# Kernel optimization log

Measured on AMD Instinct MI355X. Metric: run time of the kernel, lower is better.

Reference implementation:

```python
import jax, jax.numpy as jnp
import numpy as np

B, T, L, D, H, E, A, V = 64, 20, 196, 512, 512, 512, 512, 30000


def setup_inputs() -> dict:
    key = jax.random.key(0)
    ks = jax.random.split(key, 20)
    s = 0.02  # param init scale
    inp = {
        "captions": jax.random.randint(ks[0], (B, T), 0, V),
        "image_features": jax.random.normal(ks[1], (B, L, D), dtype=jnp.float32),
        "pooled_features": jax.random.normal(ks[2], (B, H), dtype=jnp.float32),
        "attention_mask": jnp.ones((B, L), dtype=bool),
        # embedding table
        "embedding": jax.random.normal(ks[3], (V, E), dtype=jnp.float32) * s,
        # LSTM (torch gate order i, f, g, o), input = [emb; context]
        "W_ih": jax.random.normal(ks[4], (4 * H, E + H), dtype=jnp.float32) * s,
        "W_hh": jax.random.normal(ks[5], (4 * H, H), dtype=jnp.float32) * s,
        "b_lstm": jnp.zeros((4 * H,), dtype=jnp.float32),
        # additive attention with memory/cell extra query context
        "Wq": jax.random.normal(ks[6], (H, A), dtype=jnp.float32) * s,
        "Wk": jax.random.normal(ks[7], (D, A), dtype=jnp.float32) * s,
        "Wm": jax.random.normal(ks[8], (H, A), dtype=jnp.float32) * s,
        "Wc": jax.random.normal(ks[9], (H, A), dtype=jnp.float32) * s,
        "v_att": jax.random.normal(ks[10], (A,), dtype=jnp.float32) * s,
        # output projection context(H) -> vocab
        "W_out": jax.random.normal(ks[11], (H, V), dtype=jnp.float32) * s,
        "b_out": jnp.zeros((V,), dtype=jnp.float32),
        # hidden/cell init from pooled features (num_layers = 1)
        "W_init_h": jax.random.normal(ks[12], (H, H), dtype=jnp.float32) * s,
        "b_init_h": jnp.zeros((H,), dtype=jnp.float32),
        "W_init_c": jax.random.normal(ks[13], (H, H), dtype=jnp.float32) * s,
        "b_init_c": jnp.zeros((H,), dtype=jnp.float32),
    }
    return inp


def reference(captions, image_features, pooled_features, attention_mask,
              embedding, W_ih, W_hh, b_lstm, Wq, Wk, Wm, Wc, v_att,
              W_out, b_out, W_init_h, b_init_h, W_init_c, b_init_c):
    # init hidden states from pooled features
    h0 = pooled_features @ W_init_h + b_init_h            # [B, H]
    c0 = pooled_features @ W_init_c + b_init_c            # [B, H]
    ctx0 = jnp.zeros_like(h0)                              # prev_context, [B, H]
    emb = embedding[captions]                              # [B, T, E] (dropout = eval identity)
    # precompute key projection once (hoisted out of the timestep loop)
    key_proj = jnp.einsum('bld,da->bla', image_features, Wk)  # [B, L, A]
    neg = jnp.finfo(image_features.dtype).min

    def step(carry, emb_t):
        h, c, ctx = carry
        x = jnp.concatenate([emb_t, ctx], axis=-1)         # [B, E+H]
        gates = x @ W_ih.T + h @ W_hh.T + b_lstm           # [B, 4H]
        i, f, g, o = jnp.split(gates, 4, axis=-1)
        i = jax.nn.sigmoid(i); f = jax.nn.sigmoid(f)
        g = jnp.tanh(g);       o = jax.nn.sigmoid(o)
        c_new = f * c + i * g
        h_new = o * jnp.tanh(c_new)                        # lstm output == query
        # additive attention: query + memory_state(h) + cell_state(c) context
        q = h_new @ Wq + h_new @ Wm + c_new @ Wc           # [B, A]
        scores = jnp.einsum('bla,a->bl', jnp.tanh(key_proj + q[:, None, :]), v_att)
        scores = jnp.where(attention_mask, scores, neg)
        w = jax.nn.softmax(scores, axis=-1)                # [B, L]
        ctx_new = jnp.einsum('bl,bld->bd', w, image_features)  # [B, H]
        logits_t = ctx_new @ W_out + b_out                 # [B, V]
        return (h_new, c_new, ctx_new), logits_t

    _, logits = jax.lax.scan(step, (h0, c0, ctx0), jnp.swapaxes(emb, 0, 1))
    return jnp.swapaxes(logits, 0, 1)  # [B, T, V]
```

## Files before the change

kernel.cpp:

```cpp
#include <hip/hip_runtime.h>
#include <hip/hip_bf16.h>
#include <cstdint>

#define DEV static __device__ __forceinline__

typedef __bf16 bf16;
typedef __bf16 bf16x8 __attribute__((ext_vector_type(8)));
typedef float f32x4 __attribute__((ext_vector_type(4)));

#define B_ 64
#define T_ 20
#define L_ 196
#define E_ 512
#define V_ 30000
#define VPAD 30080
#define XK 2560
#define GN 2048
#define KSPLIT 8
#define KSPAN 10

DEV float sigmoidf_(float x) { return 1.0f / (1.0f + __expf(-x)); }
DEV float tanhf_(float x) { float e = __expf(2.0f * x); return 1.0f - 2.0f / (e + 1.0f); }

DEV float ldf(const void* p, size_t i, int isbf) {
  return isbf ? (float)((const bf16*)p)[i] : ((const float*)p)[i];
}

DEV void gload_lds16(const void* g, void* l) {
  __builtin_amdgcn_global_load_lds(
      (const __attribute__((address_space(1))) void*)(uintptr_t)g,
      (__attribute__((address_space(3))) void*)(uint32_t)(uintptr_t)l,
      16, 0, 0);
}

#define WAITV4_BAR  do { asm volatile("s_waitcnt vmcnt(4)" ::: "memory"); \
                         asm volatile("s_barrier" ::: "memory"); } while (0)
#define WAITV2_BAR  do { asm volatile("s_waitcnt vmcnt(2)" ::: "memory"); \
                         asm volatile("s_barrier" ::: "memory"); } while (0)
#define WAITV0_BAR  do { asm volatile("s_waitcnt vmcnt(0)" ::: "memory"); \
                         asm volatile("s_barrier" ::: "memory"); } while (0)
#define BAR_ONLY    do { asm volatile("s_barrier" ::: "memory"); } while (0)

__global__ void k_detect(const void* __restrict__ emb, int* __restrict__ flag)
{
  if (threadIdx.x == 0) {
    const unsigned* w = (const unsigned*)emb;
    int cnt = 0;
    for (int i = 0; i < 256; ++i) {
      unsigned lo = w[i] & 0xFFFFu;
      unsigned e = (lo >> 7) & 0xFFu;
      if (e >= 100 && e <= 126) ++cnt;
    }
    *flag = (cnt >= 128) ? 1 : 0;
  }
}

__global__ __launch_bounds__(256)
void k_init_mm(const void* __restrict__ pooled, const void* __restrict__ W_init_h,
               const void* __restrict__ W_init_c, float* __restrict__ ipart,
               const int* __restrict__ flag)
{
  const int isbf = *flag;
  const int b = blockIdx.x, ks = blockIdx.y, mat = blockIdx.z;
  const void* W = mat ? W_init_c : W_init_h;
  const int tid = threadIdx.x;
  __shared__ float p_s[64];
  if (tid < 64) p_s[tid] = ldf(pooled, (size_t)b * 512 + ks * 64 + tid, isbf);
  __syncthreads();
  const int kb = ks * 64;
  float a0 = 0.0f, a1 = 0.0f;
#pragma unroll 8
  for (int k = 0; k < 64; ++k) {
    float p = p_s[k];
    a0 += p * ldf(W, (size_t)(kb + k) * 512 + tid, isbf);
    a1 += p * ldf(W, (size_t)(kb + k) * 512 + tid + 256, isbf);
  }
  float* o = ipart + (((size_t)mat * 8 + ks) * 64 + b) * 512;
  o[tid] = a0;
  o[tid + 256] = a1;
}

__global__ __launch_bounds__(256)
void k_pack(const float* __restrict__ ipart, const void* __restrict__ b_init_h,
            const void* __restrict__ b_init_c, const int* __restrict__ captions,
            const void* __restrict__ embedding, const void* __restrict__ Wq,
            const void* __restrict__ Wm, const void* __restrict__ Wc,
            bf16* __restrict__ xcomb, float* __restrict__ c_state,
            bf16* __restrict__ Wqm, bf16* __restrict__ Wcb,
            bf16* __restrict__ hc, const int* __restrict__ flag)
{
  const int isbf = *flag;
  const int tid = threadIdx.x;
  if (blockIdx.x >= 96) {
    size_t base = (size_t)(blockIdx.x - 96) * 8192;
    for (int i = tid; i < 8192; i += 256)
      Wcb[base + i] = (bf16)ldf(Wc, base + i, isbf);
    return;
  }
  if (blockIdx.x >= 64) {
    size_t base = (size_t)(blockIdx.x - 64) * 8192;
    for (int i = tid; i < 8192; i += 256)
      Wqm[base + i] = (bf16)(ldf(Wq, base + i, isbf) + ldf(Wm, base + i, isbf));
    return;
  }
  const int b = blockIdx.x;
  {
    int cap = captions[b * T_];
    for (int i = tid; i < 512; i += 256) {
      xcomb[(size_t)b * XK + i] = (bf16)ldf(embedding, (size_t)cap * E_ + i, isbf);
      xcomb[(size_t)b * XK + 512 + i]  = (bf16)0.0f;
      xcomb[(size_t)b * XK + 1024 + i] = (bf16)0.0f;
    }
  }
#pragma unroll
  for (int jj = 0; jj < 2; ++jj) {
    int j = tid + jj * 256;
    float ah = ldf(b_init_h, j, isbf), ac = ldf(b_init_c, j, isbf);
#pragma unroll
    for (int ks = 0; ks < 8; ++ks) {
      ah += ipart[(((size_t)0 * 8 + ks) * 64 + b) * 512 + j];
      ac += ipart[(((size_t)1 * 8 + ks) * 64 + b) * 512 + j];
    }
    c_state[b * 512 + j] = ac;
    bf16 hh = (bf16)ah;
    bf16 hl = (bf16)(ah - (float)hh);
    bf16 ch = (bf16)ac;
    bf16 cl = (bf16)(ac - (float)ch);
    xcomb[(size_t)b * XK + 1536 + j] = hh;
    xcomb[(size_t)b * XK + 2048 + j] = hl;
    hc[(size_t)b * 2048 + j]        = hh;
    hc[(size_t)b * 2048 + 512 + j]  = hl;
    hc[(size_t)b * 2048 + 1024 + j] = ch;
    hc[(size_t)b * 2048 + 1536 + j] = cl;
  }
}

__global__ __launch_bounds__(256)
void k_gemm(const void* __restrict__ A, const void* __restrict__ Bsrc,
            int N, int K, int kspan, int outmode, int amode, int btmode,
            float* __restrict__ outF, bf16* __restrict__ outB,
            void* __restrict__ outAny, const void* __restrict__ bias,
            const int* __restrict__ flag)
{
  const int isbf = *flag;
  const int tid  = threadIdx.x;
  const int lane = tid & 63, w = tid >> 6;
  const int n0 = blockIdx.x * 64;
  const int yt = blockIdx.y;
  const int m0 = (outmode == 1) ? 0 : yt * 64;
  const int kbase = (outmode == 1) ? yt * kspan * 32 : 0;

  __shared__ __align__(16) bf16 As[64 * 32];
  __shared__ __align__(16) bf16 Bs[64 * 32];

  f32x4 acc[2][2];
#pragma unroll
  for (int i = 0; i < 2; ++i)
#pragma unroll
    for (int j = 0; j < 2; ++j)
#pragma unroll
      for (int r = 0; r < 4; ++r) acc[i][j][r] = 0.0f;

  const int wm = (w & 1) * 32, wn = (w >> 1) * 32;
  const int sr = tid >> 2, sk = (tid & 3) * 8;
  const int fm = lane & 15, kq = (lane >> 4) * 8;
  const bool bvalid = (n0 + sr) < N;
  const int kk = tid >> 3, nn = (tid & 7) * 8;

  for (int ks = 0; ks < kspan; ++ks) {
    const size_t aidx = (size_t)(m0 + sr) * K + kbase + sk + ks * 32;
    bf16x8 av;
    if (amode == 0 || isbf) {
      av = *(const bf16x8*)((const bf16*)A + aidx);
    } else {
      const float* af = (const float*)A + aidx;
      float4 x0 = *(const float4*)af, x1 = *(const float4*)(af + 4);
      av[0] = (bf16)x0.x; av[1] = (bf16)x0.y; av[2] = (bf16)x0.z; av[3] = (bf16)x0.w;
      av[4] = (bf16)x1.x; av[5] = (bf16)x1.y; av[6] = (bf16)x1.z; av[7] = (bf16)x1.w;
    }

    if (btmode == 0) {
      bf16x8 bv;
#pragma unroll
      for (int i = 0; i < 8; ++i) bv[i] = (bf16)0.0f;
      if (bvalid)
        bv = *(const bf16x8*)((const bf16*)Bsrc + (size_t)(n0 + sr) * K + kbase + sk + ks * 32);
      __syncthreads();
      *(bf16x8*)(As + sr * 32 + sk) = av;
      *(bf16x8*)(Bs + sr * 32 + sk) = bv;
      __syncthreads();
    } else {
      float bl[8];
      const int krow = kbase + ks * 32 + kk;
#pragma unroll
      for (int i = 0; i < 8; ++i) {
        int n = n0 + nn + i;
        bl[i] = (n < N) ? ldf(Bsrc, (size_t)krow * N + n, isbf) : 0.0f;
      }
      __syncthreads();
      *(bf16x8*)(As + sr * 32 + sk) = av;
#pragma unroll
      for (int i = 0; i < 8; ++i) Bs[(nn + i) * 32 + kk] = (bf16)bl[i];
      __syncthreads();
    }

    bf16x8 a0 = *(const bf16x8*)(As + (wm + fm)      * 32 + kq);
    bf16x8 a1 = *(const bf16x8*)(As + (wm + 16 + fm) * 32 + kq);
    bf16x8 b0 = *(const bf16x8*)(Bs + (wn + fm)      * 32 + kq);
    bf16x8 b1 = *(const bf16x8*)(Bs + (wn + 16 + fm) * 32 + kq);
    acc[0][0] = __builtin_amdgcn_mfma_f32_16x16x32_bf16(a0, b0, acc[0][0], 0, 0, 0);
    acc[0][1] = __builtin_amdgcn_mfma_f32_16x16x32_bf16(a0, b1, acc[0][1], 0, 0, 0);
    acc[1][0] = __builtin_amdgcn_mfma_f32_16x16x32_bf16(a1, b0, acc[1][0], 0, 0, 0);
    acc[1][1] = __builtin_amdgcn_mfma_f32_16x16x32_bf16(a1, b1, acc[1][1], 0, 0, 0);
  }

  const int rbase = (lane >> 4) * 4;
  if (outmode == 1) {
    float* o = outF + (size_t)yt * 64 * N;
#pragma unroll
    for (int i = 0; i < 2; ++i)
#pragma unroll
      for (int j = 0; j < 2; ++j)
#pragma unroll
        for (int r = 0; r < 4; ++r) {
          int m = wm + i * 16 + rbase + r;
          int n = n0 + wn + j * 16 + fm;
          o[(size_t)m * N + n] = acc[i][j][r];
        }
  } else if (outmode == 0) {
#pragma unroll
    for (int i = 0; i < 2; ++i)
#pragma unroll
      for (int j = 0; j < 2; ++j) {
        int n = n0 + wn + j * 16 + fm;
        if (n < N) {
#pragma unroll
          for (int r = 0; r < 4; ++r) {
            int m = m0 + wm + i * 16 + rbase + r;
            outB[(size_t)m * N + n] = (bf16)acc[i][j][r];
          }
        }
      }
  } else {
#pragma unroll
    for (int i = 0; i < 2; ++i)
#pragma unroll
      for (int j = 0; j < 2; ++j) {
        int n = n0 + wn + j * 16 + fm;
        if (n < N) {
          float bb = bias ? ldf(bias, n, isbf) : 0.0f;
#pragma unroll
          for (int r = 0; r < 4; ++r) {
            int m = m0 + wm + i * 16 + rbase + r;
            float val = acc[i][j][r] + bb;
            if (isbf) ((bf16*)outAny)[(size_t)m * N + n] = (bf16)val;
            else      ((float*)outAny)[(size_t)m * N + n] = val;
          }
        }
      }
  }
}

__global__ __launch_bounds__(256)
void k_gates(const bf16* __restrict__ A, const bf16* __restrict__ BT,
             float* __restrict__ outF)
{
  const int tid = threadIdx.x, lane = tid & 63, w = tid >> 6;
  const int n0 = blockIdx.x * 64;
  const int yt = blockIdx.y;
  const int kbase = yt * KSPAN * 32;

  __shared__ __align__(16) bf16 As[2][64 * 32];
  __shared__ __align__(16) bf16 Bs[2][64 * 32];

  f32x4 acc[2][2];
#pragma unroll
  for (int i = 0; i < 2; ++i)
#pragma unroll
    for (int j = 0; j < 2; ++j)
#pragma unroll
      for (int r = 0; r < 4; ++r) acc[i][j][r] = 0.0f;

  const int wm = (w & 1) * 32, wn = (w >> 1) * 32;
  const int fm = lane & 15, kq = (lane >> 4) * 8;

  const int srow = w * 16 + (lane >> 2), skk = (lane & 3) * 8;
  const bf16* ag = A  + (size_t)srow * XK + kbase + skk;
  const bf16* bg = BT + (size_t)(n0 + srow) * XK + kbase + skk;

#define GSTAGE(cur, koff) do { \
    gload_lds16(ag + (koff), &As[cur][w * 512]); \
    gload_lds16(bg + (koff), &Bs[cur][w * 512]); } while (0)

  GSTAGE(0, 0);
  GSTAGE(1, 32);
  int cur = 0;
  for (int ks = 0; ks < KSPAN; ++ks) {
    if (ks + 1 < KSPAN) WAITV2_BAR; else WAITV0_BAR;
    bf16x8 a0 = *(const bf16x8*)(&As[cur][(wm + fm)      * 32 + kq]);
    bf16x8 a1 = *(const bf16x8*)(&As[cur][(wm + 16 + fm) * 32 + kq]);
    bf16x8 b0 = *(const bf16x8*)(&Bs[cur][(wn + fm)      * 32 + kq]);
    bf16x8 b1 = *(const bf16x8*)(&Bs[cur][(wn + 16 + fm) * 32 + kq]);
    acc[0][0] = __builtin_amdgcn_mfma_f32_16x16x32_bf16(a0, b0, acc[0][0], 0, 0, 0);
    acc[0][1] = __builtin_amdgcn_mfma_f32_16x16x32_bf16(a0, b1, acc[0][1], 0, 0, 0);
    acc[1][0] = __builtin_amdgcn_mfma_f32_16x16x32_bf16(a1, b0, acc[1][0], 0, 0, 0);
    acc[1][1] = __builtin_amdgcn_mfma_f32_16x16x32_bf16(a1, b1, acc[1][1], 0, 0, 0);
    BAR_ONLY;
    if (ks + 2 < KSPAN) GSTAGE(cur, (ks + 2) * 32);
    cur ^= 1;
  }
#undef GSTAGE

  const int rbase = (lane >> 4) * 4;
  float* o = outF + (size_t)yt * 64 * GN;
#pragma unroll
  for (int i = 0; i < 2; ++i)
#pragma unroll
    for (int j = 0; j < 2; ++j)
#pragma unroll
      for (int r = 0; r < 4; ++r) {
        int m = wm + i * 16 + rbase + r;
        int n = n0 + wn + j * 16 + fm;
        o[(size_t)m * GN + n] = acc[i][j][r];
      }
}

__global__ __launch_bounds__(256)
void k_qgemm(const bf16* __restrict__ hc, const bf16* __restrict__ WqmT,
             const bf16* __restrict__ WcbT, float* __restrict__ qpart)
{
  const int tid = threadIdx.x, lane = tid & 63, w = tid >> 6;
  const int n0 = blockIdx.x * 64;
  const int ksb = blockIdx.y;
  const int kbase = ksb * 256;
  const bf16* bsrc = (ksb < 4) ? WqmT : WcbT;
  const int kin = (ksb & 1) * 256;

  __shared__ __align__(16) bf16 As[2][64 * 32];
  __shared__ __align__(16) bf16 Bs[2][64 * 32];

  f32x4 acc[2][2];
#pragma unroll
  for (int i = 0; i < 2; ++i)
#pragma unroll
    for (int j = 0; j < 2; ++j)
#pragma unroll
      for (int r = 0; r < 4; ++r) acc[i][j][r] = 0.0f;

  const int wm = (w & 1) * 32, wn = (w >> 1) * 32;
  const int fm = lane & 15, kq = (lane >> 4) * 8;

  const int srow = w * 16 + (lane >> 2), skk = (lane & 3) * 8;
  const bf16* ag = hc   + (size_t)srow * 2048 + kbase + skk;
  const bf16* bg = bsrc + (size_t)(n0 + srow) * 512 + kin + skk;

#define QSTAGE(cur, koff) do { \
    gload_lds16(ag + (koff), &As[cur][w * 512]); \
    gload_lds16(bg + (koff), &Bs[cur][w * 512]); } while (0)

  QSTAGE(0, 0);
  QSTAGE(1, 32);
  int cur = 0;
  for (int ks = 0; ks < 8; ++ks) {
    if (ks + 1 < 8) WAITV2_BAR; else WAITV0_BAR;
    bf16x8 a0 = *(const bf16x8*)(&As[cur][(wm + fm)      * 32 + kq]);
    bf16x8 a1 = *(const bf16x8*)(&As[cur][(wm + 16 + fm) * 32 + kq]);
    bf16x8 b0 = *(const bf16x8*)(&Bs[cur][(wn + fm)      * 32 + kq]);
    bf16x8 b1 = *(const bf16x8*)(&Bs[cur][(wn + 16 + fm) * 32 + kq]);
    acc[0][0] = __builtin_amdgcn_mfma_f32_16x16x32_bf16(a0, b0, acc[0][0], 0, 0, 0);
    acc[0][1] = __builtin_amdgcn_mfma_f32_16x16x32_bf16(a0, b1, acc[0][1], 0, 0, 0);
    acc[1][0] = __builtin_amdgcn_mfma_f32_16x16x32_bf16(a1, b0, acc[1][0], 0, 0, 0);
    acc[1][1] = __builtin_amdgcn_mfma_f32_16x16x32_bf16(a1, b1, acc[1][1], 0, 0, 0);
    BAR_ONLY;
    if (ks + 2 < 8) QSTAGE(cur, (ks + 2) * 32);
    cur ^= 1;
  }
#undef QSTAGE

  const int rbase = (lane >> 4) * 4;
  float* o = qpart + (size_t)ksb * 64 * 512;
#pragma unroll
  for (int i = 0; i < 2; ++i)
#pragma unroll
    for (int j = 0; j < 2; ++j)
#pragma unroll
      for (int r = 0; r < 4; ++r) {
        int m = wm + i * 16 + rbase + r;
        int n = n0 + wn + j * 16 + fm;
        o[(size_t)m * 512 + n] = acc[i][j][r];
      }
}

__global__ __launch_bounds__(256)
void k_gemm128(const bf16* __restrict__ A, const bf16* __restrict__ BT,
               int N, int K,
               void* __restrict__ outAny, const void* __restrict__ bias,
               const int* __restrict__ flag)
{
  const int isbf = *flag;
  const int tid = threadIdx.x, lane = tid & 63, w = tid >> 6;

  const int NMT = (B_ * T_) / 128;
  const int nwg = (int)gridDim.x * (int)gridDim.y;
  const int wgid = (int)blockIdx.y * (int)gridDim.x + (int)blockIdx.x;
  const int xcd = wgid & 7, loc = wgid >> 3;
  const int qq = nwg >> 3, rr = nwg & 7;
  const int swz = (xcd < rr ? xcd * (qq + 1) : rr * (qq + 1) + (xcd - rr) * qq) + loc;
  const int n0 = (swz / NMT) * 128, m0 = (swz % NMT) * 128;

  __shared__ __align__(16) bf16 As[2][128 * 32];
  __shared__ __align__(16) bf16 Bs[2][128 * 32];

  f32x4 acc[4][4];
#pragma unroll
  for (int i = 0; i < 4; ++i)
#pragma unroll
    for (int j = 0; j < 4; ++j)
#pragma unroll
      for (int r = 0; r < 4; ++r) acc[i][j][r] = 0.0f;

  const int lr = lane >> 2;
  const int lk = (lane & 3) * 8;
  const int fm = lane & 15, kq = (lane >> 4) * 8;
  const int wm = (w & 1) * 64, wn = (w >> 1) * 64;
  const int li0 = w * 2, li1 = w * 2 + 1;

  const bf16* a0g = A  + (size_t)(m0 + li0 * 16 + lr) * K + lk;
  const bf16* a1g = A  + (size_t)(m0 + li1 * 16 + lr) * K + lk;
  const bf16* b0g = BT + (size_t)(n0 + li0 * 16 + lr) * K + lk;
  const bf16* b1g = BT + (size_t)(n0 + li1 * 16 + lr) * K + lk;

#define STAGE128(cur, koff) do { \
    gload_lds16(a0g + (koff), &As[cur][li0 * 512]); \
    gload_lds16(a1g + (koff), &As[cur][li1 * 512]); \
    gload_lds16(b0g + (koff), &Bs[cur][li0 * 512]); \
    gload_lds16(b1g + (koff), &Bs[cur][li1 * 512]); } while (0)

  const int kiters = K >> 5;
  STAGE128(0, 0);
  STAGE128(1, 32);
  int cur = 0;
  for (int ks = 0; ks < kiters; ++ks) {
    if (ks + 1 < kiters) WAITV4_BAR; else WAITV0_BAR;
    bf16x8 af[4], bf[4];
#pragma unroll
    for (int i = 0; i < 4; ++i) {
      af[i] = *(const bf16x8*)(&As[cur][(wm + i * 16 + fm) * 32 + kq]);
      bf[i] = *(const bf16x8*)(&Bs[cur][(wn + i * 16 + fm) * 32 + kq]);
    }
#pragma unroll
    for (int i = 0; i < 4; ++i)
#pragma unroll
      for (int j = 0; j < 4; ++j)
        acc[i][j] = __builtin_amdgcn_mfma_f32_16x16x32_bf16(af[i], bf[j], acc[i][j], 0, 0, 0);
    BAR_ONLY;
    if (ks + 2 < kiters) STAGE128(cur, (ks + 2) * 32);
    cur ^= 1;
  }
#undef STAGE128

  const int rbase = (lane >> 4) * 4;
#pragma unroll
  for (int j = 0; j < 4; ++j) {
    int n = n0 + wn + j * 16 + fm;
    if (n < N) {
      float bb = bias ? ldf(bias, n, isbf) : 0.0f;
#pragma unroll
      for (int i = 0; i < 4; ++i)
#pragma unroll
        for (int r = 0; r < 4; ++r) {
          int m = m0 + wm + i * 16 + rbase + r;
          float val = acc[i][j][r] + bb;
          if (isbf) ((bf16*)outAny)[(size_t)m * N + n] = (bf16)val;
          else      ((float*)outAny)[(size_t)m * N + n] = val;
        }
    }
  }
}

__global__ __launch_bounds__(256)
void k_transpose(const void* __restrict__ in, bf16* __restrict__ out, int R, int C,
                 int Cpad, const int* __restrict__ flag)
{
  const int isbf = *flag;
  __shared__ bf16 tile[32][33];
  const int c0 = blockIdx.x * 32, r0 = blockIdx.y * 32;
  const int cc = threadIdx.x & 31, rw = threadIdx.x >> 5;
#pragma unroll
  for (int s = 0; s < 4; ++s) {
    int r = r0 + rw + s * 8, c = c0 + cc;
    tile[rw + s * 8][cc] = (r < R && c < C) ? (bf16)ldf(in, (size_t)r * C + c, isbf)
                                            : (bf16)0.0f;
  }
  __syncthreads();
#pragma unroll
  for (int s = 0; s < 4; ++s) {
    int c = c0 + rw + s * 8, r = r0 + cc;
    if (c < Cpad && r < R) out[(size_t)c * R + r] = tile[cc][rw + s * 8];
  }
}

__global__ __launch_bounds__(256)
void k_transpose_bf(const bf16* __restrict__ in, bf16* __restrict__ out)
{
  __shared__ bf16 tile[32][33];
  const int c0 = blockIdx.x * 32, r0 = blockIdx.y * 32;
  const int cc = threadIdx.x & 31, rw = threadIdx.x >> 5;
#pragma unroll
  for (int s = 0; s < 4; ++s)
    tile[rw + s * 8][cc] = in[(size_t)(r0 + rw + s * 8) * 512 + c0 + cc];
  __syncthreads();
#pragma unroll
  for (int s = 0; s < 4; ++s)
    out[(size_t)(c0 + rw + s * 8) * 512 + r0 + cc] = tile[cc][rw + s * 8];
}

__global__ __launch_bounds__(256)
void k_buildWcomb(const void* __restrict__ W_ih, const void* __restrict__ W_hh,
                  bf16* __restrict__ WcombT, const int* __restrict__ flag)
{
  const int isbf = *flag;
  const int n = blockIdx.x;
  for (int k = threadIdx.x; k < XK; k += 256) {
    float v;
    if (k < 512)       v = ldf(W_ih, (size_t)n * 1024 + k, isbf);
    else if (k < 1536) v = ldf(W_ih, (size_t)n * 1024 + 512 + ((k - 512) & 511), isbf);
    else               v = ldf(W_hh, (size_t)n * 512 + ((k - 1536) & 511), isbf);
    WcombT[(size_t)n * XK + k] = (bf16)v;
  }
}

__global__ __launch_bounds__(512)
void k_lstm(const float* __restrict__ partials, const void* __restrict__ b_lstm,
            float* __restrict__ c_state, bf16* __restrict__ xcomb,
            bf16* __restrict__ hc, const int* __restrict__ flag)
{
  const int isbf = *flag;
  const int b = blockIdx.x, j = threadIdx.x;
  float g4[4];
#pragma unroll
  for (int g = 0; g < 4; ++g) {
    int gc = g * 512 + j;
    float s = ldf(b_lstm, gc, isbf);
#pragma unroll
    for (int sp = 0; sp < KSPLIT; ++sp)
      s += partials[((size_t)sp * 64 + b) * 2048 + gc];
    g4[g] = s;
  }
  float ig = sigmoidf_(g4[0]);
  float fg = sigmoidf_(g4[1]);
  float gg = tanhf_(g4[2]);
  float og = sigmoidf_(g4[3]);
  float cn = fg * c_state[b * 512 + j] + ig * gg;
  float hn = og * tanhf_(cn);
  c_state[b * 512 + j] = cn;
  bf16 hh = (bf16)hn;
  bf16 hl = (bf16)(hn - (float)hh);
  bf16 ch = (bf16)cn;
  bf16 cl = (bf16)(cn - (float)ch);
  xcomb[(size_t)b * XK + 1536 + j] = hh;
  xcomb[(size_t)b * XK + 2048 + j] = hl;
  hc[(size_t)b * 2048 + j]        = hh;
  hc[(size_t)b * 2048 + 512 + j]  = hl;
  hc[(size_t)b * 2048 + 1024 + j] = ch;
  hc[(size_t)b * 2048 + 1536 + j] = cl;
}

__global__ __launch_bounds__(1024)
void k_attn(const float* __restrict__ qpart, const bf16* __restrict__ keyproj,
            const void* __restrict__ v_att, const void* __restrict__ img,
            bf16* __restrict__ xcomb, bf16* __restrict__ ctx_all,
            const int* __restrict__ captions, const void* __restrict__ embedding,
            int t, const int* __restrict__ flag)
{
  const int isbf = *flag;
  const int b = blockIdx.x, dq = blockIdx.y, tid = threadIdx.x;
  __shared__ float q_s[512];
  __shared__ float sc_s[256];
  __shared__ float wred[32];
  __shared__ float red[64 * 128];

  if (tid < 512) {
    float s = 0.0f;
#pragma unroll
    for (int ks = 0; ks < 8; ++ks)
      s += qpart[((size_t)ks * 64 + b) * 512 + tid];
    q_s[tid] = s;
  }
  __syncthreads();

  {
    const int wv = tid >> 6, ln = tid & 63;
    float q8[8], v8[8];
#pragma unroll
    for (int i = 0; i < 8; ++i) {
      q8[i] = q_s[ln * 8 + i];
      v8[i] = ldf(v_att, ln * 8 + i, isbf);
    }
    for (int l = wv; l < 196; l += 16) {
      bf16x8 kv = *(const bf16x8*)(keyproj + ((size_t)b * 196 + l) * 512 + ln * 8);
      float s = 0.0f;
#pragma unroll
      for (int i = 0; i < 8; ++i)
        s += tanhf_((float)kv[i] + q8[i]) * v8[i];
      s += __shfl_xor(s, 32); s += __shfl_xor(s, 16); s += __shfl_xor(s, 8);
      s += __shfl_xor(s, 4);  s += __shfl_xor(s, 2);  s += __shfl_xor(s, 1);
      if (ln == 0) sc_s[l] = s;
    }
  }
  __syncthreads();

  {
    const int wv = tid >> 6, ln = tid & 63;
    float v = (tid < 196) ? sc_s[tid] : -3.0e38f;
    float m = v;
    m = fmaxf(m, __shfl_xor(m, 32)); m = fmaxf(m, __shfl_xor(m, 16));
    m = fmaxf(m, __shfl_xor(m, 8));  m = fmaxf(m, __shfl_xor(m, 4));
    m = fmaxf(m, __shfl_xor(m, 2));  m = fmaxf(m, __shfl_xor(m, 1));
    if (ln == 0) wred[wv] = m;
    __syncthreads();
    m = wred[0];
#pragma unroll
    for (int i = 1; i < 16; ++i) m = fmaxf(m, wred[i]);
    float e = (tid < 196) ? __expf(v - m) : 0.0f;
    float ss = e;
    ss += __shfl_xor(ss, 32); ss += __shfl_xor(ss, 16); ss += __shfl_xor(ss, 8);
    ss += __shfl_xor(ss, 4);  ss += __shfl_xor(ss, 2);  ss += __shfl_xor(ss, 1);
    if (ln == 0) wred[16 + wv] = ss;
    __syncthreads();
    float tot = 0.0f;
#pragma unroll
    for (int i = 0; i < 16; ++i) tot += wred[16 + i];
    if (tid < 196) sc_s[tid] = e / tot;
  }
  __syncthreads();

  {
    const int worker = tid >> 4;
    const int d8 = (tid & 15) * 8;
    const int dcol = dq * 128 + d8;
    float cx[8];
#pragma unroll
    for (int i = 0; i < 8; ++i) cx[i] = 0.0f;
    if (isbf) {
      for (int l = worker; l < 196; l += 64) {
        float wl = sc_s[l];
        bf16x8 iv = *(const bf16x8*)((const bf16*)img + ((size_t)b * 196 + l) * 512 + dcol);
#pragma unroll
        for (int i = 0; i < 8; ++i) cx[i] += wl * (float)iv[i];
      }
    } else {
      for (int l = worker; l < 196; l += 64) {
        float wl = sc_s[l];
        const float* ip = (const float*)img + ((size_t)b * 196 + l) * 512 + dcol;
        float4 x0 = *(const float4*)ip, x1 = *(const float4*)(ip + 4);
        cx[0] += wl * x0.x; cx[1] += wl * x0.y; cx[2] += wl * x0.z; cx[3] += wl * x0.w;
        cx[4] += wl * x1.x; cx[5] += wl * x1.y; cx[6] += wl * x1.z; cx[7] += wl * x1.w;
      }
    }
#pragma unroll
    for (int i = 0; i < 8; ++i) red[worker * 128 + d8 + i] = cx[i];
  }
  __syncthreads();
  if (tid < 128) {
    float s = 0.0f;
#pragma unroll 8
    for (int w64 = 0; w64 < 64; ++w64) s += red[w64 * 128 + tid];
    const int d = dq * 128 + tid;
    bf16 ch = (bf16)s;
    xcomb[(size_t)b * XK + 512 + d]  = ch;
    xcomb[(size_t)b * XK + 1024 + d] = (bf16)(s - (float)ch);
    ctx_all[((size_t)b * T_ + t) * 512 + d] = ch;
  }

  if (dq == 3 && t + 1 < T_) {
    int cap = captions[b * T_ + t + 1];
    for (int i = tid; i < 512; i += 1024)
      xcomb[(size_t)b * XK + i] = (bf16)ldf(embedding, (size_t)cap * E_ + i, isbf);
  }
}

extern "C" void kernel_launch(void* const* d_in, const int* in_sizes, int n_in,
                              void* d_out, int out_size, void* d_ws, size_t ws_size,
                              hipStream_t stream)
{
  (void)in_sizes; (void)n_in; (void)out_size;
  const int*  captions  = (const int*)d_in[0];
  const void* img       = d_in[1];
  const void* pooled    = d_in[2];
  const void* embedding = d_in[4];
  const void* W_ih      = d_in[5];
  const void* W_hh      = d_in[6];
  const void* b_lstm    = d_in[7];
  const void* Wq        = d_in[8];
  const void* Wk        = d_in[9];
  const void* Wm        = d_in[10];
  const void* Wc        = d_in[11];
  const void* v_att     = d_in[12];
  const void* W_out     = d_in[13];
  const void* b_out     = d_in[14];
  const void* W_init_h  = d_in[15];
  const void* b_init_h  = d_in[16];
  const void* W_init_c  = d_in[17];
  const void* b_init_c  = d_in[18];

  char* ws = (char*)d_ws;
  size_t off = 0;
  auto alloc = [&](size_t bytes) {
    void* p = ws + off;
    off += (bytes + 255) & ~(size_t)255;
    return p;
  };
  int*   flag     = (int*)alloc(256);
  bf16*  xcomb    = (bf16*)alloc((size_t)B_ * XK * 2);
  float* c_state  = (float*)alloc((size_t)B_ * 512 * 4);
  bf16*  ctx_all  = (bf16*)alloc((size_t)B_ * T_ * 512 * 2);
  bf16*  Wqm      = (bf16*)alloc((size_t)512 * 512 * 2);
  bf16*  Wcb      = (bf16*)alloc((size_t)512 * 512 * 2);
  bf16*  WkT      = (bf16*)alloc((size_t)512 * 512 * 2);
  float* partials = (float*)alloc((size_t)KSPLIT * B_ * GN * 4);
  bf16*  keyproj  = (bf16*)alloc((size_t)B_ * L_ * 512 * 2);
  bf16*  WcombT   = (bf16*)alloc((size_t)GN * XK * 2);
  bf16*  hc       = (bf16*)alloc((size_t)B_ * 2048 * 2);
  bf16*  WqmT     = (bf16*)alloc((size_t)512 * 512 * 2);
  bf16*  WcbT     = (bf16*)alloc((size_t)512 * 512 * 2);
  bf16*  WoutT    = (bf16*)alloc((size_t)VPAD * 512 * 2);
  const bool fits = (off <= ws_size);
  float* ipart = partials;
  float* qpart = partials;

  k_detect<<<1, 64, 0, stream>>>(embedding, flag);
  k_init_mm<<<dim3(64, 8, 2), 256, 0, stream>>>(pooled, W_init_h, W_init_c, ipart, flag);
  k_pack<<<128, 256, 0, stream>>>(ipart, b_init_h, b_init_c, captions, embedding,
                                  Wq, Wm, Wc, xcomb, c_state, Wqm, Wcb, hc, flag);
  k_buildWcomb<<<GN, 256, 0, stream>>>(W_ih, W_hh, WcombT, flag);
  k_transpose<<<dim3(16, 16), 256, 0, stream>>>(Wk, WkT, 512, 512, 512, flag);
  k_transpose_bf<<<dim3(16, 16), 256, 0, stream>>>(Wqm, WqmT);
  k_transpose_bf<<<dim3(16, 16), 256, 0, stream>>>(Wcb, WcbT);
  if (fits)
    k_transpose<<<dim3(VPAD / 32, 16), 256, 0, stream>>>(W_out, WoutT, 512, V_, VPAD, flag);

  k_gemm<<<dim3(8, L_ * B_ / 64), 256, 0, stream>>>(
      img, WkT, 512, 512, 16, 0, 1, 0,
      nullptr, keyproj, nullptr, nullptr, flag);

  for (int t = 0; t < T_; ++t) {
    k_gates<<<dim3(GN / 64, KSPLIT), 256, 0, stream>>>(xcomb, WcombT, partials);
    k_lstm<<<B_, 512, 0, stream>>>(partials, b_lstm, c_state, xcomb, hc, flag);
    k_qgemm<<<dim3(8, 8), 256, 0, stream>>>(hc, WqmT, WcbT, qpart);
    k_attn<<<dim3(B_, 4), 1024, 0, stream>>>(qpart, keyproj, v_att, img,
                                             xcomb, ctx_all, captions, embedding,
                                             t, flag);
  }

  if (fits) {
    k_gemm128<<<dim3(VPAD / 128, B_ * T_ / 128), 256, 0, stream>>>(
        ctx_all, WoutT, V_, 512, d_out, b_out, flag);
  } else {
    k_gemm<<<dim3((V_ + 63) / 64, B_ * T_ / 64), 256, 0, stream>>>(
        ctx_all, W_out, V_, 512, 16, 2, 0, 1,
        nullptr, nullptr, d_out, b_out, flag);
  }
}
```

Before: 1.247 ms.

## Fuse per-timestep recurrent kernels into one persistent kernel with grid barriers

The loop of 20 timesteps used to launch four kernels per step: gates GEMM, LSTM cell, query GEMM and attention. All of that now runs inside one persistent 256-block kernel that separates the phases with an atomic-counter grid barrier. The aim is to remove about 80 kernel launches and their launch gaps from the serial recurrence. In exchange it adds four spin-wait grid barriers per step, idles many blocks in the smaller phases, and relies on all 256 blocks being resident at once, or the kernel will deadlock. The tile GEMMs are reshaped so that half of each 512-thread block loads the A operand and the other half loads B.

```diff
diff --git a/kernel.cpp b/kernel.cpp
--- a/kernel.cpp
+++ b/kernel.cpp
@@ -18,6 +18,7 @@
 #define GN 2048
 #define KSPLIT 8
 #define KSPAN 10
+#define NBLK 256
 
 DEV float sigmoidf_(float x) { return 1.0f / (1.0f + __expf(-x)); }
 DEV float tanhf_(float x) { float e = __expf(2.0f * x); return 1.0f - 2.0f / (e + 1.0f); }
@@ -33,15 +34,31 @@
       16, 0, 0);
 }
 
-#define WAITV4_BAR  do { asm volatile("s_waitcnt vmcnt(4)" ::: "memory"); \
+#define WAITV1_BAR  do { asm volatile("s_waitcnt vmcnt(1)" ::: "memory"); \
                          asm volatile("s_barrier" ::: "memory"); } while (0)
 #define WAITV2_BAR  do { asm volatile("s_waitcnt vmcnt(2)" ::: "memory"); \
+                         asm volatile("s_barrier" ::: "memory"); } while (0)
+#define WAITV4_BAR  do { asm volatile("s_waitcnt vmcnt(4)" ::: "memory"); \
                          asm volatile("s_barrier" ::: "memory"); } while (0)
 #define WAITV0_BAR  do { asm volatile("s_waitcnt vmcnt(0)" ::: "memory"); \
                          asm volatile("s_barrier" ::: "memory"); } while (0)
 #define BAR_ONLY    do { asm volatile("s_barrier" ::: "memory"); } while (0)
 
-__global__ void k_detect(const void* __restrict__ emb, int* __restrict__ flag)
+DEV void gridbar(int* cnt) {
+  __syncthreads();
+  if (threadIdx.x == 0) {
+    int ticket = __hip_atomic_fetch_add(cnt, 1, __ATOMIC_ACQ_REL,
+                                        __HIP_MEMORY_SCOPE_AGENT);
+    int target = (ticket / NBLK + 1) * NBLK;
+    while (__hip_atomic_load(cnt, __ATOMIC_ACQUIRE,
+                             __HIP_MEMORY_SCOPE_AGENT) < target)
+      __builtin_amdgcn_s_sleep(1);
+  }
+  __syncthreads();
+}
+
+__global__ void k_detect(const void* __restrict__ emb, int* __restrict__ flag,
+                         int* __restrict__ gcnt)
 {
   if (threadIdx.x == 0) {
     const unsigned* w = (const unsigned*)emb;
@@ -52,6 +69,7 @@
       if (e >= 100 && e <= 126) ++cnt;
     }
     *flag = (cnt >= 128) ? 1 : 0;
+    *gcnt = 0;
   }
 }
 
@@ -87,7 +105,7 @@
             const void* __restrict__ Wm, const void* __restrict__ Wc,
             bf16* __restrict__ xcomb, float* __restrict__ c_state,
             bf16* __restrict__ Wqm, bf16* __restrict__ Wcb,
-            bf16* __restrict__ hc, const int* __restrict__ flag)
+            const int* __restrict__ flag)
 {
   const int isbf = *flag;
   const int tid = threadIdx.x;
@@ -123,15 +141,8 @@
     }
     c_state[b * 512 + j] = ac;
     bf16 hh = (bf16)ah;
-    bf16 hl = (bf16)(ah - (float)hh);
-    bf16 ch = (bf16)ac;
-    bf16 cl = (bf16)(ac - (float)ch);
     xcomb[(size_t)b * XK + 1536 + j] = hh;
-    xcomb[(size_t)b * XK + 2048 + j] = hl;
-    hc[(size_t)b * 2048 + j]        = hh;
-    hc[(size_t)b * 2048 + 512 + j]  = hl;
-    hc[(size_t)b * 2048 + 1024 + j] = ch;
-    hc[(size_t)b * 2048 + 1536 + j] = cl;
+    xcomb[(size_t)b * XK + 2048 + j] = (bf16)(ah - (float)hh);
   }
 }
 
@@ -262,136 +273,6 @@
 }
 
 __global__ __launch_bounds__(256)
-void k_gates(const bf16* __restrict__ A, const bf16* __restrict__ BT,
-             float* __restrict__ outF)
-{
-  const int tid = threadIdx.x, lane = tid & 63, w = tid >> 6;
-  const int n0 = blockIdx.x * 64;
-  const int yt = blockIdx.y;
-  const int kbase = yt * KSPAN * 32;
-
-  __shared__ __align__(16) bf16 As[2][64 * 32];
-  __shared__ __align__(16) bf16 Bs[2][64 * 32];
-
-  f32x4 acc[2][2];
-#pragma unroll
-  for (int i = 0; i < 2; ++i)
-#pragma unroll
-    for (int j = 0; j < 2; ++j)
-#pragma unroll
-      for (int r = 0; r < 4; ++r) acc[i][j][r] = 0.0f;
-
-  const int wm = (w & 1) * 32, wn = (w >> 1) * 32;
-  const int fm = lane & 15, kq = (lane >> 4) * 8;
-
-  const int srow = w * 16 + (lane >> 2), skk = (lane & 3) * 8;
-  const bf16* ag = A  + (size_t)srow * XK + kbase + skk;
-  const bf16* bg = BT + (size_t)(n0 + srow) * XK + kbase + skk;
-
-#define GSTAGE(cur, koff) do { \
-    gload_lds16(ag + (koff), &As[cur][w * 512]); \
-    gload_lds16(bg + (koff), &Bs[cur][w * 512]); } while (0)
-
-  GSTAGE(0, 0);
-  GSTAGE(1, 32);
-  int cur = 0;
-  for (int ks = 0; ks < KSPAN; ++ks) {
-    if (ks + 1 < KSPAN) WAITV2_BAR; else WAITV0_BAR;
-    bf16x8 a0 = *(const bf16x8*)(&As[cur][(wm + fm)      * 32 + kq]);
-    bf16x8 a1 = *(const bf16x8*)(&As[cur][(wm + 16 + fm) * 32 + kq]);
-    bf16x8 b0 = *(const bf16x8*)(&Bs[cur][(wn + fm)      * 32 + kq]);
-    bf16x8 b1 = *(const bf16x8*)(&Bs[cur][(wn + 16 + fm) * 32 + kq]);
-    acc[0][0] = __builtin_amdgcn_mfma_f32_16x16x32_bf16(a0, b0, acc[0][0], 0, 0, 0);
-    acc[0][1] = __builtin_amdgcn_mfma_f32_16x16x32_bf16(a0, b1, acc[0][1], 0, 0, 0);
-    acc[1][0] = __builtin_amdgcn_mfma_f32_16x16x32_bf16(a1, b0, acc[1][0], 0, 0, 0);
-    acc[1][1] = __builtin_amdgcn_mfma_f32_16x16x32_bf16(a1, b1, acc[1][1], 0, 0, 0);
-    BAR_ONLY;
-    if (ks + 2 < KSPAN) GSTAGE(cur, (ks + 2) * 32);
-    cur ^= 1;
-  }
-#undef GSTAGE
-
-  const int rbase = (lane >> 4) * 4;
-  float* o = outF + (size_t)yt * 64 * GN;
-#pragma unroll
-  for (int i = 0; i < 2; ++i)
-#pragma unroll
-    for (int j = 0; j < 2; ++j)
-#pragma unroll
-      for (int r = 0; r < 4; ++r) {
-        int m = wm + i * 16 + rbase + r;
-        int n = n0 + wn + j * 16 + fm;
-        o[(size_t)m * GN + n] = acc[i][j][r];
-      }
-}
-
-__global__ __launch_bounds__(256)
-void k_qgemm(const bf16* __restrict__ hc, const bf16* __restrict__ WqmT,
-             const bf16* __restrict__ WcbT, float* __restrict__ qpart)
-{
-  const int tid = threadIdx.x, lane = tid & 63, w = tid >> 6;
-  const int n0 = blockIdx.x * 64;
-  const int ksb = blockIdx.y;
-  const int kbase = ksb * 256;
-  const bf16* bsrc = (ksb < 4) ? WqmT : WcbT;
-  const int kin = (ksb & 1) * 256;
-
-  __shared__ __align__(16) bf16 As[2][64 * 32];
-  __shared__ __align__(16) bf16 Bs[2][64 * 32];
-
-  f32x4 acc[2][2];
-#pragma unroll
-  for (int i = 0; i < 2; ++i)
-#pragma unroll
-    for (int j = 0; j < 2; ++j)
-#pragma unroll
-      for (int r = 0; r < 4; ++r) acc[i][j][r] = 0.0f;
-
-  const int wm = (w & 1) * 32, wn = (w >> 1) * 32;
-  const int fm = lane & 15, kq = (lane >> 4) * 8;
-
-  const int srow = w * 16 + (lane >> 2), skk = (lane & 3) * 8;
-  const bf16* ag = hc   + (size_t)srow * 2048 + kbase + skk;
-  const bf16* bg = bsrc + (size_t)(n0 + srow) * 512 + kin + skk;
-
-#define QSTAGE(cur, koff) do { \
-    gload_lds16(ag + (koff), &As[cur][w * 512]); \
-    gload_lds16(bg + (koff), &Bs[cur][w * 512]); } while (0)
-
-  QSTAGE(0, 0);
-  QSTAGE(1, 32);
-  int cur = 0;
-  for (int ks = 0; ks < 8; ++ks) {
-    if (ks + 1 < 8) WAITV2_BAR; else WAITV0_BAR;
-    bf16x8 a0 = *(const bf16x8*)(&As[cur][(wm + fm)      * 32 + kq]);
-    bf16x8 a1 = *(const bf16x8*)(&As[cur][(wm + 16 + fm) * 32 + kq]);
-    bf16x8 b0 = *(const bf16x8*)(&Bs[cur][(wn + fm)      * 32 + kq]);
-    bf16x8 b1 = *(const bf16x8*)(&Bs[cur][(wn + 16 + fm) * 32 + kq]);
-    acc[0][0] = __builtin_amdgcn_mfma_f32_16x16x32_bf16(a0, b0, acc[0][0], 0, 0, 0);
-    acc[0][1] = __builtin_amdgcn_mfma_f32_16x16x32_bf16(a0, b1, acc[0][1], 0, 0, 0);
-    acc[1][0] = __builtin_amdgcn_mfma_f32_16x16x32_bf16(a1, b0, acc[1][0], 0, 0, 0);
-    acc[1][1] = __builtin_amdgcn_mfma_f32_16x16x32_bf16(a1, b1, acc[1][1], 0, 0, 0);
-    BAR_ONLY;
-    if (ks + 2 < 8) QSTAGE(cur, (ks + 2) * 32);
-    cur ^= 1;
-  }
-#undef QSTAGE
-
-  const int rbase = (lane >> 4) * 4;
-  float* o = qpart + (size_t)ksb * 64 * 512;
-#pragma unroll
-  for (int i = 0; i < 2; ++i)
-#pragma unroll
-    for (int j = 0; j < 2; ++j)
-#pragma unroll
-      for (int r = 0; r < 4; ++r) {
-        int m = wm + i * 16 + rbase + r;
-        int n = n0 + wn + j * 16 + fm;
-        o[(size_t)m * 512 + n] = acc[i][j][r];
-      }
-}
-
-__global__ __launch_bounds__(256)
 void k_gemm128(const bf16* __restrict__ A, const bf16* __restrict__ BT,
                int N, int K,
                void* __restrict__ outAny, const void* __restrict__ bias,
@@ -530,153 +411,229 @@
   }
 }
 
+DEV void gemm64_run(const bf16* gsrc, bf16* As, bf16* Bs, bool isA, int wq,
+                    int kspan, int wm, int wn, int fm, int kq,
+                    f32x4& acc0, f32x4& acc1)
+{
+  bf16* dbuf = isA ? As : Bs;
+  gload_lds16(gsrc,      dbuf + wq);
+  gload_lds16(gsrc + 32, dbuf + 2048 + wq);
+  int cur = 0;
+  for (int ks = 0; ks < kspan; ++ks) {
+    if (ks + 1 < kspan) WAITV1_BAR; else WAITV0_BAR;
+    const bf16* Ac = As + cur * 2048;
+    const bf16* Bc = Bs + cur * 2048;
+    bf16x8 a0 = *(const bf16x8*)(Ac + (wm + fm)      * 32 + kq);
+    bf16x8 a1 = *(const bf16x8*)(Ac + (wm + 16 + fm) * 32 + kq);
+    bf16x8 b0 = *(const bf16x8*)(Bc + (wn + fm)      * 32 + kq);
+    acc0 = __builtin_amdgcn_mfma_f32_16x16x32_bf16(a0, b0, acc0, 0, 0, 0);
+    acc1 = __builtin_amdgcn_mfma_f32_16x16x32_bf16(a1, b0, acc1, 0, 0, 0);
+    BAR_ONLY;
+    if (ks + 2 < kspan) gload_lds16(gsrc + (ks + 2) * 32, dbuf + cur * 2048 + wq);
+    cur ^= 1;
+  }
+}
+
 __global__ __launch_bounds__(512)
-void k_lstm(const float* __restrict__ partials, const void* __restrict__ b_lstm,
-            float* __restrict__ c_state, bf16* __restrict__ xcomb,
-            bf16* __restrict__ hc, const int* __restrict__ flag)
-{
+void k_loop(bf16* __restrict__ xcomb, const bf16* __restrict__ WcombT,
+            float* __restrict__ partials, const void* __restrict__ b_lstm,
+            float* __restrict__ c_state, bf16* __restrict__ hc,
+            const bf16* __restrict__ WqmT, const bf16* __restrict__ WcbT,
+            float* __restrict__ qpart, const bf16* __restrict__ keyproj,
+            const void* __restrict__ v_att, const void* __restrict__ img,
+            bf16* __restrict__ ctx_all, const int* __restrict__ captions,
+            const void* __restrict__ embedding, int* __restrict__ gcnt,
+            const int* __restrict__ flag)
+{
+  __shared__ __align__(16) union {
+    struct { bf16 As[2][2048]; bf16 Bs[2][2048]; } g;
+    struct { float q_s[512]; float sc_s[256]; float wred[16];
+             float red[32 * 128]; } a;
+  } sm;
+
   const int isbf = *flag;
-  const int b = blockIdx.x, j = threadIdx.x;
-  float g4[4];
-#pragma unroll
-  for (int g = 0; g < 4; ++g) {
-    int gc = g * 512 + j;
-    float s = ldf(b_lstm, gc, isbf);
-#pragma unroll
-    for (int sp = 0; sp < KSPLIT; ++sp)
-      s += partials[((size_t)sp * 64 + b) * 2048 + gc];
-    g4[g] = s;
-  }
-  float ig = sigmoidf_(g4[0]);
-  float fg = sigmoidf_(g4[1]);
-  float gg = tanhf_(g4[2]);
-  float og = sigmoidf_(g4[3]);
-  float cn = fg * c_state[b * 512 + j] + ig * gg;
-  float hn = og * tanhf_(cn);
-  c_state[b * 512 + j] = cn;
-  bf16 hh = (bf16)hn;
-  bf16 hl = (bf16)(hn - (float)hh);
-  bf16 ch = (bf16)cn;
-  bf16 cl = (bf16)(cn - (float)ch);
-  xcomb[(size_t)b * XK + 1536 + j] = hh;
-  xcomb[(size_t)b * XK + 2048 + j] = hl;
-  hc[(size_t)b * 2048 + j]        = hh;
-  hc[(size_t)b * 2048 + 512 + j]  = hl;
-  hc[(size_t)b * 2048 + 1024 + j] = ch;
-  hc[(size_t)b * 2048 + 1536 + j] = cl;
-}
-
-__global__ __launch_bounds__(1024)
-void k_attn(const float* __restrict__ qpart, const bf16* __restrict__ keyproj,
-            const void* __restrict__ v_att, const void* __restrict__ img,
-            bf16* __restrict__ xcomb, bf16* __restrict__ ctx_all,
-            const int* __restrict__ captions, const void* __restrict__ embedding,
-            int t, const int* __restrict__ flag)
-{
-  const int isbf = *flag;
-  const int b = blockIdx.x, dq = blockIdx.y, tid = threadIdx.x;
-  __shared__ float q_s[512];
-  __shared__ float sc_s[256];
-  __shared__ float wred[32];
-  __shared__ float red[64 * 128];
-
-  if (tid < 512) {
-    float s = 0.0f;
-#pragma unroll
-    for (int ks = 0; ks < 8; ++ks)
-      s += qpart[((size_t)ks * 64 + b) * 512 + tid];
-    q_s[tid] = s;
-  }
-  __syncthreads();
-
-  {
-    const int wv = tid >> 6, ln = tid & 63;
-    float q8[8], v8[8];
-#pragma unroll
-    for (int i = 0; i < 8; ++i) {
-      q8[i] = q_s[ln * 8 + i];
-      v8[i] = ldf(v_att, ln * 8 + i, isbf);
-    }
-    for (int l = wv; l < 196; l += 16) {
-      bf16x8 kv = *(const bf16x8*)(keyproj + ((size_t)b * 196 + l) * 512 + ln * 8);
-      float s = 0.0f;
-#pragma unroll
-      for (int i = 0; i < 8; ++i)
-        s += tanhf_((float)kv[i] + q8[i]) * v8[i];
-      s += __shfl_xor(s, 32); s += __shfl_xor(s, 16); s += __shfl_xor(s, 8);
-      s += __shfl_xor(s, 4);  s += __shfl_xor(s, 2);  s += __shfl_xor(s, 1);
-      if (ln == 0) sc_s[l] = s;
-    }
-  }
-  __syncthreads();
-
-  {
-    const int wv = tid >> 6, ln = tid & 63;
-    float v = (tid < 196) ? sc_s[tid] : -3.0e38f;
-    float m = v;
-    m = fmaxf(m, __shfl_xor(m, 32)); m = fmaxf(m, __shfl_xor(m, 16));
-    m = fmaxf(m, __shfl_xor(m, 8));  m = fmaxf(m, __shfl_xor(m, 4));
-    m = fmaxf(m, __shfl_xor(m, 2));  m = fmaxf(m, __shfl_xor(m, 1));
-    if (ln == 0) wred[wv] = m;
-    __syncthreads();
-    m = wred[0];
-#pragma unroll
-    for (int i = 1; i < 16; ++i) m = fmaxf(m, wred[i]);
-    float e = (tid < 196) ? __expf(v - m) : 0.0f;
-    float ss = e;
-    ss += __shfl_xor(ss, 32); ss += __shfl_xor(ss, 16); ss += __shfl_xor(ss, 8);
-    ss += __shfl_xor(ss, 4);  ss += __shfl_xor(ss, 2);  ss += __shfl_xor(ss, 1);
-    if (ln == 0) wred[16 + wv] = ss;
-    __syncthreads();
-    float tot = 0.0f;
-#pragma unroll
-    for (int i = 0; i < 16; ++i) tot += wred[16 + i];
-    if (tid < 196) sc_s[tid] = e / tot;
-  }
-  __syncthreads();
-
-  {
-    const int worker = tid >> 4;
-    const int d8 = (tid & 15) * 8;
-    const int dcol = dq * 128 + d8;
-    float cx[8];
-#pragma unroll
-    for (int i = 0; i < 8; ++i) cx[i] = 0.0f;
-    if (isbf) {
-      for (int l = worker; l < 196; l += 64) {
-        float wl = sc_s[l];
-        bf16x8 iv = *(const bf16x8*)((const bf16*)img + ((size_t)b * 196 + l) * 512 + dcol);
-#pragma unroll
-        for (int i = 0; i < 8; ++i) cx[i] += wl * (float)iv[i];
-      }
-    } else {
-      for (int l = worker; l < 196; l += 64) {
-        float wl = sc_s[l];
-        const float* ip = (const float*)img + ((size_t)b * 196 + l) * 512 + dcol;
-        float4 x0 = *(const float4*)ip, x1 = *(const float4*)(ip + 4);
-        cx[0] += wl * x0.x; cx[1] += wl * x0.y; cx[2] += wl * x0.z; cx[3] += wl * x0.w;
-        cx[4] += wl * x1.x; cx[5] += wl * x1.y; cx[6] += wl * x1.z; cx[7] += wl * x1.w;
-      }
-    }
-#pragma unroll
-    for (int i = 0; i < 8; ++i) red[worker * 128 + d8 + i] = cx[i];
-  }
-  __syncthreads();
-  if (tid < 128) {
-    float s = 0.0f;
+  const int bid = blockIdx.x, tid = threadIdx.x;
+  const int lane = tid & 63, w = tid >> 6;
+  const int fm = lane & 15, kq = (lane >> 4) * 8;
+  const int rbase = (lane >> 4) * 4;
+  const int wm = (w >> 2) * 32, wn = (w & 3) * 16;
+  const int wq = (w & 3) * 512;
+  const int s = tid & 255;
+  const int srow = s >> 2, skk = (s & 3) * 8;
+  const bool isA = (tid < 256);
+
+  for (int t = 0; t < T_; ++t) {
+    {
+      const int nt = bid & 31, yt = bid >> 5;
+      const int n0 = nt * 64, kbase = yt * KSPAN * 32;
+      const bf16* gsrc = isA
+          ? xcomb  + (size_t)srow * XK + kbase + skk
+          : WcombT + (size_t)(n0 + srow) * XK + kbase + skk;
+      f32x4 acc0, acc1;
+#pragma unroll
+      for (int r = 0; r < 4; ++r) { acc0[r] = 0.0f; acc1[r] = 0.0f; }
+      gemm64_run(gsrc, &sm.g.As[0][0], &sm.g.Bs[0][0], isA, wq, KSPAN,
+                 wm, wn, fm, kq, acc0, acc1);
+      float* o = partials + (size_t)yt * 64 * GN;
+      const int n = n0 + wn + fm;
+#pragma unroll
+      for (int r = 0; r < 4; ++r) {
+        o[(size_t)(wm + rbase + r) * GN + n]      = acc0[r];
+        o[(size_t)(wm + 16 + rbase + r) * GN + n] = acc1[r];
+      }
+    }
+    gridbar(gcnt);
+
+    if (bid < 64) {
+      const int b = bid, j = tid;
+      float g4[4];
+#pragma unroll
+      for (int g = 0; g < 4; ++g) {
+        int gc = g * 512 + j;
+        float sacc = ldf(b_lstm, gc, isbf);
+#pragma unroll
+        for (int sp = 0; sp < KSPLIT; ++sp)
+          sacc += partials[((size_t)sp * 64 + b) * 2048 + gc];
+        g4[g] = sacc;
+      }
+      float ig = sigmoidf_(g4[0]);
+      float fg = sigmoidf_(g4[1]);
+      float gg = tanhf_(g4[2]);
+      float og = sigmoidf_(g4[3]);
+      float cn = fg * c_state[b * 512 + j] + ig * gg;
+      float hn = og * tanhf_(cn);
+      c_state[b * 512 + j] = cn;
+      bf16 hh = (bf16)hn;
+      bf16 hl = (bf16)(hn - (float)hh);
+      bf16 ch = (bf16)cn;
+      bf16 cl = (bf16)(cn - (float)ch);
+      xcomb[(size_t)b * XK + 1536 + j] = hh;
+      xcomb[(size_t)b * XK + 2048 + j] = hl;
+      hc[(size_t)b * 2048 + j]        = hh;
+      hc[(size_t)b * 2048 + 512 + j]  = hl;
+      hc[(size_t)b * 2048 + 1024 + j] = ch;
+      hc[(size_t)b * 2048 + 1536 + j] = cl;
+    }
+    gridbar(gcnt);
+
+    if (bid < 64) {
+      const int nt = bid & 7, ksb = bid >> 3;
+      const int n0 = nt * 64, kbase = ksb * 256;
+      const bf16* bsrc = (ksb < 4) ? WqmT : WcbT;
+      const int kin = (ksb & 1) * 256;
+      const bf16* gsrc = isA
+          ? hc   + (size_t)srow * 2048 + kbase + skk
+          : bsrc + (size_t)(n0 + srow) * 512 + kin + skk;
+      f32x4 acc0, acc1;
+#pragma unroll
+      for (int r = 0; r < 4; ++r) { acc0[r] = 0.0f; acc1[r] = 0.0f; }
+      gemm64_run(gsrc, &sm.g.As[0][0], &sm.g.Bs[0][0], isA, wq, 8,
+                 wm, wn, fm, kq, acc0, acc1);
+      float* o = qpart + (size_t)ksb * 64 * 512;
+      const int n = n0 + wn + fm;
+#pragma unroll
+      for (int r = 0; r < 4; ++r) {
+        o[(size_t)(wm + rbase + r) * 512 + n]      = acc0[r];
+        o[(size_t)(wm + 16 + rbase + r) * 512 + n] = acc1[r];
+      }
+    }
+    gridbar(gcnt);
+
+    {
+      const int b = bid >> 2, dq = bid & 3;
+      {
+        float qs = 0.0f;
+#pragma unroll
+        for (int ks = 0; ks < 8; ++ks)
+          qs += qpart[((size_t)ks * 64 + b) * 512 + tid];
+        sm.a.q_s[tid] = qs;
+      }
+      __syncthreads();
+      {
+        float q8[8], v8[8];
+#pragma unroll
+        for (int i = 0; i < 8; ++i) {
+          q8[i] = sm.a.q_s[lane * 8 + i];
+          v8[i] = ldf(v_att, lane * 8 + i, isbf);
+        }
+        for (int l = w; l < 196; l += 8) {
+          bf16x8 kv = *(const bf16x8*)(keyproj + ((size_t)b * 196 + l) * 512 + lane * 8);
+          float sc = 0.0f;
+#pragma unroll
+          for (int i = 0; i < 8; ++i)
+            sc += tanhf_((float)kv[i] + q8[i]) * v8[i];
+          sc += __shfl_xor(sc, 32); sc += __shfl_xor(sc, 16); sc += __shfl_xor(sc, 8);
+          sc += __shfl_xor(sc, 4);  sc += __shfl_xor(sc, 2);  sc += __shfl_xor(sc, 1);
+          if (lane == 0) sm.a.sc_s[l] = sc;
+        }
+      }
+      __syncthreads();
+      {
+        float v = (tid < 196) ? sm.a.sc_s[tid] : -3.0e38f;
+        float m = v;
+        m = fmaxf(m, __shfl_xor(m, 32)); m = fmaxf(m, __shfl_xor(m, 16));
+        m = fmaxf(m, __shfl_xor(m, 8));  m = fmaxf(m, __shfl_xor(m, 4));
+        m = fmaxf(m, __shfl_xor(m, 2));  m = fmaxf(m, __shfl_xor(m, 1));
+        if (lane == 0) sm.a.wred[w] = m;
+        __syncthreads();
+        m = sm.a.wred[0];
+#pragma unroll
+        for (int i = 1; i < 8; ++i) m = fmaxf(m, sm.a.wred[i]);
+        float e = (tid < 196) ? __expf(v - m) : 0.0f;
+        float ss = e;
+        ss += __shfl_xor(ss, 32); ss += __shfl_xor(ss, 16); ss += __shfl_xor(ss, 8);
+        ss += __shfl_xor(ss, 4);  ss += __shfl_xor(ss, 2);  ss += __shfl_xor(ss, 1);
+        if (lane == 0) sm.a.wred[8 + w] = ss;
+        __syncthreads();
+        float tot = 0.0f;
+#pragma unroll
+        for (int i = 0; i < 8; ++i) tot += sm.a.wred[8 + i];
+        if (tid < 196) sm.a.sc_s[tid] = e / tot;
+      }
+      __syncthreads();
+      {
+        const int worker = tid >> 4;
+        const int d8 = (tid & 15) * 8;
+        const int dcol = dq * 128 + d8;
+        float cx[8];
+#pragma unroll
+        for (int i = 0; i < 8; ++i) cx[i] = 0.0f;
+        if (isbf) {
+          for (int l = worker; l < 196; l += 32) {
+            float wl = sm.a.sc_s[l];
+            bf16x8 iv = *(const bf16x8*)((const bf16*)img + ((size_t)b * 196 + l) * 512 + dcol);
+#pragma unroll
+            for (int i = 0; i < 8; ++i) cx[i] += wl * (float)iv[i];
+          }
+        } else {
+          for (int l = worker; l < 196; l += 32) {
+            float wl = sm.a.sc_s[l];
+            const float* ip = (const float*)img + ((size_t)b * 196 + l) * 512 + dcol;
+            float4 x0 = *(const float4*)ip, x1 = *(const float4*)(ip + 4);
+            cx[0] += wl * x0.x; cx[1] += wl * x0.y; cx[2] += wl * x0.z; cx[3] += wl * x0.w;
+            cx[4] += wl * x1.x; cx[5] += wl * x1.y; cx[6] += wl * x1.z; cx[7] += wl * x1.w;
+          }
+        }
+#pragma unroll
+        for (int i = 0; i < 8; ++i) sm.a.red[worker * 128 + d8 + i] = cx[i];
+      }
+      __syncthreads();
+      if (tid < 128) {
+        float sacc = 0.0f;
 #pragma unroll 8
-    for (int w64 = 0; w64 < 64; ++w64) s += red[w64 * 128 + tid];
-    const int d = dq * 128 + tid;
-    bf16 ch = (bf16)s;
-    xcomb[(size_t)b * XK + 512 + d]  = ch;
-    xcomb[(size_t)b * XK + 1024 + d] = (bf16)(s - (float)ch);
-    ctx_all[((size_t)b * T_ + t) * 512 + d] = ch;
-  }
-
-  if (dq == 3 && t + 1 < T_) {
-    int cap = captions[b * T_ + t + 1];
-    for (int i = tid; i < 512; i += 1024)
-      xcomb[(size_t)b * XK + i] = (bf16)ldf(embedding, (size_t)cap * E_ + i, isbf);
+        for (int w32 = 0; w32 < 32; ++w32) sacc += sm.a.red[w32 * 128 + tid];
+        const int d = dq * 128 + tid;
+        bf16 ch = (bf16)sacc;
+        xcomb[(size_t)b * XK + 512 + d]  = ch;
+        xcomb[(size_t)b * XK + 1024 + d] = (bf16)(sacc - (float)ch);
+        ctx_all[((size_t)b * T_ + t) * 512 + d] = ch;
+      }
+      if (dq == 3 && t + 1 < T_) {
+        int cap = captions[b * T_ + t + 1];
+        xcomb[(size_t)b * XK + tid] = (bf16)ldf(embedding, (size_t)cap * E_ + tid, isbf);
+      }
+    }
+    gridbar(gcnt);
   }
 }
 
@@ -712,6 +669,7 @@
     return p;
   };
   int*   flag     = (int*)alloc(256);
+  int*   gcnt     = (int*)alloc(256);
   bf16*  xcomb    = (bf16*)alloc((size_t)B_ * XK * 2);
   float* c_state  = (float*)alloc((size_t)B_ * 512 * 4);
   bf16*  ctx_all  = (bf16*)alloc((size_t)B_ * T_ * 512 * 2);
@@ -729,10 +687,10 @@
   float* ipart = partials;
   float* qpart = partials;
 
-  k_detect<<<1, 64, 0, stream>>>(embedding, flag);
+  k_detect<<<1, 64, 0, stream>>>(embedding, flag, gcnt);
   k_init_mm<<<dim3(64, 8, 2), 256, 0, stream>>>(pooled, W_init_h, W_init_c, ipart, flag);
   k_pack<<<128, 256, 0, stream>>>(ipart, b_init_h, b_init_c, captions, embedding,
-                                  Wq, Wm, Wc, xcomb, c_state, Wqm, Wcb, hc, flag);
+                                  Wq, Wm, Wc, xcomb, c_state, Wqm, Wcb, flag);
   k_buildWcomb<<<GN, 256, 0, stream>>>(W_ih, W_hh, WcombT, flag);
   k_transpose<<<dim3(16, 16), 256, 0, stream>>>(Wk, WkT, 512, 512, 512, flag);
   k_transpose_bf<<<dim3(16, 16), 256, 0, stream>>>(Wqm, WqmT);
@@ -744,14 +702,9 @@
       img, WkT, 512, 512, 16, 0, 1, 0,
       nullptr, keyproj, nullptr, nullptr, flag);
 
-  for (int t = 0; t < T_; ++t) {
-    k_gates<<<dim3(GN / 64, KSPLIT), 256, 0, stream>>>(xcomb, WcombT, partials);
-    k_lstm<<<B_, 512, 0, stream>>>(partials, b_lstm, c_state, xcomb, hc, flag);
-    k_qgemm<<<dim3(8, 8), 256, 0, stream>>>(hc, WqmT, WcbT, qpart);
-    k_attn<<<dim3(B_, 4), 1024, 0, stream>>>(qpart, keyproj, v_att, img,
-                                             xcomb, ctx_all, captions, embedding,
-                                             t, flag);
-  }
+  k_loop<<<NBLK, 512, 0, stream>>>(xcomb, WcombT, partials, b_lstm, c_state, hc,
+                                   WqmT, WcbT, qpart, keyproj, v_att, img,
+                                   ctx_all, captions, embedding, gcnt, flag);
 
   if (fits) {
     k_gemm128<<<dim3(VPAD / 128, B_ * T_ / 128), 256, 0, stream>>>(
```

Result: slower. 2.744 ms (+120.1%).
